# Optimization experiments

Hardware: AMD Instinct MI355X
Metric: run time of the kernel (lower is better)

The kernel has to match this reference:

```python
import jax, jax.numpy as jnp
import numpy as np

N_NODES = 50000
N_EDGES = 800000
OUT_DIM = 394
BN_EPS = 1e-5


def setup_inputs() -> dict:
    key = jax.random.key(0)
    ks = jax.random.split(key, 10)
    x = jax.random.normal(ks[0], (N_NODES, 2), dtype=jnp.float32)
    edge_index = jax.random.randint(ks[1], (2, N_EDGES), 0, N_NODES, dtype=jnp.int64)
    W_gcn = jax.random.normal(ks[2], (OUT_DIM, 2), dtype=jnp.float32) * 0.5
    b_gcn = jax.random.normal(ks[3], (OUT_DIM,), dtype=jnp.float32) * 0.1
    bn_gamma = jax.random.normal(ks[4], (OUT_DIM,), dtype=jnp.float32) * 0.1 + 1.0
    bn_beta = jax.random.normal(ks[5], (OUT_DIM,), dtype=jnp.float32) * 0.1
    bn_mean = jax.random.normal(ks[6], (OUT_DIM,), dtype=jnp.float32) * 0.1
    bn_var = jax.random.uniform(ks[7], (OUT_DIM,), dtype=jnp.float32, minval=0.5, maxval=1.5)
    fc_w = jax.random.normal(ks[8], (OUT_DIM, OUT_DIM), dtype=jnp.float32) * (1.0 / np.sqrt(OUT_DIM))
    fc_b = jax.random.normal(ks[9], (OUT_DIM,), dtype=jnp.float32) * 0.1
    return {"x": x, "edge_index": edge_index, "W_gcn": W_gcn, "b_gcn": b_gcn,
            "bn_gamma": bn_gamma, "bn_beta": bn_beta, "bn_mean": bn_mean,
            "bn_var": bn_var, "fc_w": fc_w, "fc_b": fc_b}


def reference(x, edge_index, W_gcn, b_gcn, bn_gamma, bn_beta, bn_mean, bn_var, fc_w, fc_b):
    n = x.shape[0]
    loop = jnp.arange(n, dtype=edge_index.dtype)
    # PyG GCNConv: add self-loops, symmetric deg^{-1/2} normalization
    src = jnp.concatenate([edge_index[0], loop])  # [E+N] message sources
    dst = jnp.concatenate([edge_index[1], loop])  # [E+N] message targets
    deg = jax.ops.segment_sum(jnp.ones_like(dst, dtype=x.dtype), dst, num_segments=n)
    dinv = jnp.where(deg > 0, jax.lax.rsqrt(deg), 0.0)
    norm = dinv[src] * dinv[dst]  # [E+N]
    xl = x @ W_gcn.T  # [N, 394] linear transform before aggregation
    msgs = xl[src] * norm[:, None]  # [E+N, 394] gathered + normalized messages
    agg = jax.ops.segment_sum(msgs, dst, num_segments=n) + b_gcn  # scatter-add
    h = jax.nn.relu(agg)
    # BatchNorm1d in eval mode (running stats)
    h = (h - bn_mean) * jax.lax.rsqrt(bn_var + BN_EPS) * bn_gamma + bn_beta
    # dropout is a no-op in eval mode
    z = h @ fc_w.T + fc_b
    return (jax.nn.log_softmax(z, axis=1), z)
```

## Files before the change

### kernel.cpp

```cpp
#include <hip/hip_runtime.h>
#include <math.h>

#define DIM 394
#define KP  416
#define NT  13
#define NP  448
#define BN_EPS 1e-5f
#define MAXD 32
#define TST 452

typedef __bf16 bf16x8 __attribute__((ext_vector_type(8)));
typedef float  f32x4  __attribute__((ext_vector_type(4)));

__device__ inline bool edges_are_int32(const int* ei) {
    int l = threadIdx.x & 63;
    unsigned long long b = __ballot(ei[2 * l + 1] != 0);
    return b != 0ULL;
}


__global__ void prep_kernel(const float* __restrict__ Wg, const float* __restrict__ bg,
                            const float* __restrict__ gamma, const float* __restrict__ beta,
                            const float* __restrict__ mean, const float* __restrict__ var,
                            const float* __restrict__ fcw,
                            uint4* __restrict__ zbase, float4* __restrict__ Pk,
                            float* __restrict__ Ok, bf16x8* __restrict__ Bp,
                            int z4, int zb) {
    int b = blockIdx.x, t = threadIdx.x;
    if (b < zb) {
        int i = b * 256 + t;
        if (i < z4) zbase[i] = make_uint4(0u, 0u, 0u, 0u);
    } else if (b < zb + 2) {
        int k = (b - zb) * 256 + t;
        if (k < KP) {
            float4 p = make_float4(0.f, 0.f, 0.f, 0.f);
            float o = 0.f;
            if (k < DIM) {
                p.x = Wg[2 * k];
                p.y = Wg[2 * k + 1];
                p.z = bg[k];
                float sc = gamma[k] * rsqrtf(var[k] + BN_EPS);
                p.w = sc;
                o = beta[k] - sc * mean[k];
            }
            Pk[k] = p;
            Ok[k] = o;
        }
    } else {
        int idx = (b - zb - 2) * 256 + t;
        if (idx < NT * 4 * NP) {
            int col = idx % NP;
            int r   = idx / NP;
            int k0  = r * 8;
            bf16x8 v;
            #pragma unroll
            for (int q = 0; q < 8; ++q) {
                int k = k0 + q;
                float f = (col < DIM && k < DIM) ? fcw[col * DIM + k] : 0.0f;
                v[q] = (__bf16)f;
            }
            Bp[idx] = v;
        }
    }
}

__global__ void place_kernel(const int* __restrict__ ei,
                             unsigned* __restrict__ degc,
                             unsigned* __restrict__ payload,
                             unsigned* __restrict__ ocnt,
                             uint2* __restrict__ olist, int e) {
    bool is32 = edges_are_int32(ei);
    int i0 = (blockIdx.x * blockDim.x + threadIdx.x) * 16;
    if (i0 >= e) return;
    int s[16], d[16];
    int cnt = 16;
    if (i0 + 16 <= e && (e & 15) == 0) {
        if (is32) {
            #pragma unroll
            for (int v = 0; v < 4; ++v) {
                int4 a = *reinterpret_cast<const int4*>(&ei[i0 + 4 * v]);
                int4 c = *reinterpret_cast<const int4*>(&ei[e + i0 + 4 * v]);
                s[4*v] = a.x; s[4*v+1] = a.y; s[4*v+2] = a.z; s[4*v+3] = a.w;
                d[4*v] = c.x; d[4*v+1] = c.y; d[4*v+2] = c.z; d[4*v+3] = c.w;
            }
        } else {
            #pragma unroll
            for (int v = 0; v < 8; ++v) {
                int4 a = *reinterpret_cast<const int4*>(&ei[2 * i0 + 4 * v]);
                int4 c = *reinterpret_cast<const int4*>(&ei[2 * (e + i0) + 4 * v]);
                s[2*v] = a.x; s[2*v+1] = a.z;
                d[2*v] = c.x; d[2*v+1] = c.z;
            }
        }
    } else {
        cnt = e - i0 < 16 ? e - i0 : 16;
        for (int j = 0; j < cnt; ++j) {
            s[j] = is32 ? ei[i0 + j]     : ei[2 * (i0 + j)];
            d[j] = is32 ? ei[e + i0 + j] : ei[2 * (e + i0 + j)];
        }
    }
    #pragma unroll
    for (int j = 0; j < 16; ++j) {
        if (j >= cnt) break;
        unsigned tk = atomicAdd(&degc[d[j]], 1u);
        if (tk < MAXD) {
            payload[(size_t)d[j] * MAXD + tk] = (unsigned)s[j];
        } else {
            unsigned o = atomicAdd(ocnt, 1u);
            olist[o] = make_uint2((unsigned)s[j], (unsigned)d[j]);
        }
    }
}

__global__ void xs_cleanup_kernel(const float2* __restrict__ x2,
                                  const unsigned* __restrict__ degc,
                                  float2* __restrict__ xs2,
                                  const uint2* __restrict__ olist,
                                  const unsigned* __restrict__ ocnt,
                                  float* __restrict__ yover, int n, int nb0) {
    int b = blockIdx.x;
    if (b < nb0) {
        int i = b * 256 + threadIdx.x;
        if (i < n) {
            float di = rsqrtf(1.0f + (float)degc[i]);
            float2 xv = x2[i];
            xs2[i] = make_float2(di * xv.x, di * xv.y);
        }
    } else {
        unsigned cnt = *ocnt;
        unsigned t = (b - nb0) * 256 + threadIdx.x;
        for (unsigned i = t; i < cnt; i += 512) {
            uint2 sd = olist[i];
            float ds = rsqrtf(1.0f + (float)degc[sd.x]);
            float2 xv = x2[sd.x];
            atomicAdd(&yover[2 * sd.y],     ds * xv.x);
            atomicAdd(&yover[2 * sd.y + 1], ds * xv.y);
        }
    }
}

__global__ __launch_bounds__(256, 2)
void gemm_fused(const float2* __restrict__ xs2, const unsigned* __restrict__ degc,
                const unsigned* __restrict__ payload, const float* __restrict__ yover,
                const float4* __restrict__ PkG, const float* __restrict__ OkG,
                const bf16x8* __restrict__ Bp, const float* __restrict__ fcb,
                float* __restrict__ outp, float* __restrict__ z, int n) {
    __shared__ alignas(16) char smem[16 * TST * 4 + 64];
    bf16x8* As   = (bf16x8*)smem;
    float2* red  = (float2*)(smem + 8192);
    float4* PkL  = (float4*)(smem + 10240);
    float*  OkL  = (float*)(smem + 16896);
    float*  T    = (float*)smem;
    float*  lsebuf = (float*)(smem + 16 * TST * 4);

    int tid = threadIdx.x;
    int wv  = tid >> 6;
    int l   = tid & 63;
    int cg_ = tid & 15;
    int kg  = l >> 4;
    int row0 = blockIdx.x * 64;
    int gi = row0 + l;

    for (int i = tid; i < KP; i += 256) {
        PkL[i] = PkG[i];
        OkL[i] = OkG[i];
    }

    float y0 = 0.f, y1 = 0.f;
    {
        float2 psum = make_float2(0.f, 0.f);
        float dinv_i = 0.f;
        float2 xsg = make_float2(0.f, 0.f);
        if (gi < n) {
            unsigned dg = degc[gi];
            dinv_i = rsqrtf(1.0f + (float)dg);
            xsg = xs2[gi];
            unsigned m = dg < MAXD ? dg : MAXD;
            const unsigned* pl = payload + (size_t)gi * MAXD;
            for (unsigned t = wv; t < m; t += 4) {
                float2 xv = xs2[pl[t]];
                psum.x += xv.x;
                psum.y += xv.y;
            }
            if (wv == 0) {
                psum.x += yover[2 * gi];
                psum.y += yover[2 * gi + 1];
            }
        }
        red[l * 4 + wv] = psum;
        __syncthreads();
        if (gi < n) {
            float sx = red[l * 4 + 0].x + red[l * 4 + 1].x + red[l * 4 + 2].x + red[l * 4 + 3].x;
            float sy = red[l * 4 + 0].y + red[l * 4 + 1].y + red[l * 4 + 2].y + red[l * 4 + 3].y;
            y0 = dinv_i * (sx + xsg.x);
            y1 = dinv_i * (sy + xsg.y);
        }
    }

    f32x4 acc[4][7];
    #pragma unroll
    for (int a = 0; a < 4; ++a)
        #pragma unroll
        for (int b = 0; b < 7; ++b)
            acc[a][b] = (f32x4){0.f, 0.f, 0.f, 0.f};

    auto stageA = [&](int ks, int buf) {
        int kb = ks * 32 + wv * 8;
        bf16x8 hv;
        #pragma unroll
        for (int q = 0; q < 8; ++q) {
            float4 p = PkL[kb + q];
            float t = fmaf(y0, p.x, fmaf(y1, p.y, p.z));
            t = fmaxf(t, 0.f);
            hv[q] = (__bf16)fmaf(p.w, t, OkL[kb + q]);
        }
        As[buf * 256 + wv * 64 + l] = hv;
    };

    const bf16x8* bptr = Bp + (kg * 448 + wv * 112 + cg_);

    bf16x8 Bcur[7], Bnxt[7];
    #pragma unroll
    for (int c = 0; c < 7; ++c) Bcur[c] = bptr[c * 16];
    stageA(0, 0);
    __syncthreads();

    int buf = 0;
    for (int ks = 0; ks < NT; ++ks) {
        if (ks < NT - 1) {
            const bf16x8* bn = bptr + (size_t)(ks + 1) * (4 * 448);
            #pragma unroll
            for (int c = 0; c < 7; ++c) Bnxt[c] = bn[c * 16];
            stageA(ks + 1, buf ^ 1);
        }
        bf16x8 af[4];
        #pragma unroll
        for (int rt = 0; rt < 4; ++rt)
            af[rt] = As[buf * 256 + kg * 64 + rt * 16 + cg_];
        #pragma unroll
        for (int ct = 0; ct < 7; ++ct)
            #pragma unroll
            for (int rt = 0; rt < 4; ++rt)
                acc[rt][ct] = __builtin_amdgcn_mfma_f32_16x16x32_bf16(
                                  af[rt], Bcur[ct], acc[rt][ct], 0, 0, 0);
        __syncthreads();
        #pragma unroll
        for (int c = 0; c < 7; ++c) Bcur[c] = Bnxt[c];
        buf ^= 1;
    }

    float* redm = (float*)smem;
    float* reds = redm + 256;

    int colb = wv * 112;
    float bias[7];
    bool  cv[7];
    #pragma unroll
    for (int ct = 0; ct < 7; ++ct) {
        int c = colb + ct * 16 + cg_;
        cv[ct] = (c < DIM);
        bias[ct] = cv[ct] ? fcb[c] : 0.f;
    }
    #pragma unroll
    for (int rt = 0; rt < 4; ++rt)
        #pragma unroll
        for (int ct = 0; ct < 7; ++ct)
            acc[rt][ct] = acc[rt][ct] + bias[ct];

    f32x4 mx[4];
    #pragma unroll
    for (int rt = 0; rt < 4; ++rt) {
        f32x4 m = (f32x4){-1e30f, -1e30f, -1e30f, -1e30f};
        #pragma unroll
        for (int ct = 0; ct < 7; ++ct) {
            if (!cv[ct]) continue;
            #pragma unroll
            for (int j = 0; j < 4; ++j) m[j] = fmaxf(m[j], acc[rt][ct][j]);
        }
        #pragma unroll
        for (int msk = 1; msk < 16; msk <<= 1)
            #pragma unroll
            for (int j = 0; j < 4; ++j)
                m[j] = fmaxf(m[j], __shfl_xor(m[j], msk));
        mx[rt] = m;
    }
    __syncthreads();
    if (cg_ == 0) {
        #pragma unroll
        for (int rt = 0; rt < 4; ++rt)
            #pragma unroll
            for (int j = 0; j < 4; ++j)
                redm[(rt * 16 + kg * 4 + j) * 4 + wv] = mx[rt][j];
    }
    __syncthreads();
    f32x4 gm[4];
    #pragma unroll
    for (int rt = 0; rt < 4; ++rt)
        #pragma unroll
        for (int j = 0; j < 4; ++j) {
            int r = (rt * 16 + kg * 4 + j) * 4;
            gm[rt][j] = fmaxf(fmaxf(redm[r], redm[r + 1]),
                              fmaxf(redm[r + 2], redm[r + 3]));
        }

    f32x4 sm[4];
    #pragma unroll
    for (int rt = 0; rt < 4; ++rt) {
        f32x4 s = (f32x4){0.f, 0.f, 0.f, 0.f};
        #pragma unroll
        for (int ct = 0; ct < 7; ++ct) {
            if (!cv[ct]) continue;
            #pragma unroll
            for (int j = 0; j < 4; ++j)
                s[j] += __expf(acc[rt][ct][j] - gm[rt][j]);
        }
        #pragma unroll
        for (int msk = 1; msk < 16; msk <<= 1)
            #pragma unroll
            for (int j = 0; j < 4; ++j)
                s[j] += __shfl_xor(s[j], msk);
        sm[rt] = s;
    }
    if (cg_ == 0) {
        #pragma unroll
        for (int rt = 0; rt < 4; ++rt)
            #pragma unroll
            for (int j = 0; j < 4; ++j)
                reds[(rt * 16 + kg * 4 + j) * 4 + wv] = sm[rt][j];
    }
    __syncthreads();
    f32x4 lse[4];
    #pragma unroll
    for (int rt = 0; rt < 4; ++rt)
        #pragma unroll
        for (int j = 0; j < 4; ++j) {
            int r = (rt * 16 + kg * 4 + j) * 4;
            float t = reds[r] + reds[r + 1] + reds[r + 2] + reds[r + 3];
            lse[rt][j] = gm[rt][j] + __logf(t);
        }
    __syncthreads();

    #pragma unroll
    for (int rt = 0; rt < 4; ++rt) {
        #pragma unroll
        for (int ct = 0; ct < 7; ++ct) {
            int c = colb + ct * 16 + cg_;
            #pragma unroll
            for (int j = 0; j < 4; ++j)
                T[(kg * 4 + j) * TST + c] = acc[rt][ct][j];
        }
        if (wv == 0 && cg_ == 0) {
            #pragma unroll
            for (int j = 0; j < 4; ++j)
                lsebuf[kg * 4 + j] = lse[rt][j];
        }
        __syncthreads();
        #pragma unroll
        for (int q = 0; q < 7; ++q) {
            int idx = tid + q * 256;
            int row = idx / 112;
            int c4  = idx - row * 112;
            int grow2 = row0 + rt * 16 + row;
            if (grow2 < n && c4 <= 98) {
                float4 v = *reinterpret_cast<const float4*>(&T[row * TST + c4 * 4]);
                float L = lsebuf[row];
                size_t base = (size_t)grow2 * DIM + c4 * 4;
                if (c4 <= 97) {
                    *reinterpret_cast<float2*>(&z[base])        = make_float2(v.x, v.y);
                    *reinterpret_cast<float2*>(&z[base + 2])    = make_float2(v.z, v.w);
                    *reinterpret_cast<float2*>(&outp[base])     = make_float2(v.x - L, v.y - L);
                    *reinterpret_cast<float2*>(&outp[base + 2]) = make_float2(v.z - L, v.w - L);
                } else {
                    *reinterpret_cast<float2*>(&z[base])    = make_float2(v.x, v.y);
                    *reinterpret_cast<float2*>(&outp[base]) = make_float2(v.x - L, v.y - L);
                }
            }
        }
        __syncthreads();
    }
}

extern "C" void kernel_launch(void* const* d_in, const int* in_sizes, int n_in,
                              void* d_out, int out_size, void* d_ws, size_t ws_size,
                              hipStream_t stream) {
    int n = in_sizes[0] / 2;
    int e = in_sizes[1] / 2;

    const float2* x2   = (const float2*)d_in[0];
    const int*   ei    = (const int*)d_in[1];
    const float* Wg    = (const float*)d_in[2];
    const float* bg    = (const float*)d_in[3];
    const float* gamma = (const float*)d_in[4];
    const float* beta  = (const float*)d_in[5];
    const float* mean  = (const float*)d_in[6];
    const float* var   = (const float*)d_in[7];
    const float* fcw   = (const float*)d_in[8];
    const float* fcb   = (const float*)d_in[9];

    float* out = (float*)d_out;
    float* z   = out + (size_t)n * DIM;

    char* wsb = (char*)d_ws;
    unsigned* degc  = (unsigned*)wsb;
    float*    yover = (float*)(degc + n);
    unsigned* ocnt  = (unsigned*)(yover + 2 * (size_t)n);
    float2*   xs2   = (float2*)(ocnt + 4);
    uint2*    olist = (uint2*)(xs2 + n);
    size_t off = (size_t)(5 * n + 4) * 4 + (size_t)e * 8;
    off = (off + 255) & ~(size_t)255;
    unsigned* payload = (unsigned*)(wsb + off);
    off += (size_t)n * MAXD * 4;
    off = (off + 255) & ~(size_t)255;
    bf16x8* Bp = (bf16x8*)(wsb + off);
    off += (size_t)NT * 4 * NP * 16;
    float4* Pk = (float4*)(wsb + off);
    off += (size_t)KP * 16;
    float* Ok  = (float*)(wsb + off);

    int zwords = 3 * n + 4;
    int z4 = (zwords + 3) / 4;
    int zb = (z4 + 255) / 256;
    int prep_blocks = zb + 2 + (NT * 4 * NP + 255) / 256;
    int eb16 = (e / 16 + 255) / 256 + 1;
    int nb0 = (n + 255) / 256;

    prep_kernel<<<prep_blocks, 256, 0, stream>>>(Wg, bg, gamma, beta, mean, var,
                                                 fcw, (uint4*)degc, Pk, Ok, Bp,
                                                 z4, zb);
    place_kernel<<<eb16, 256, 0, stream>>>(ei, degc, payload, ocnt, olist, e);
    xs_cleanup_kernel<<<nb0 + 2, 256, 0, stream>>>(x2, degc, xs2, olist, ocnt,
                                                   yover, n, nb0);

    int gm = (n + 63) / 64;
    gemm_fused<<<gm, 256, 0, stream>>>(xs2, degc, payload, yover,
                                       Pk, Ok, Bp, fcb, out, z, n);
}
```

Baseline: 115.3 us.

## Shrink GEMM row tile to 32 rows and raise occupancy to four blocks per CU

The fused GCN+FC kernel now handles 32 rows per block instead of 64, halving accumulator registers, and launch bounds ask for 4 blocks per CU instead of 2. Neighbor aggregation is split across 8 partial sums per row, and A staging writes bf16x4 halves. The B register double-buffer is dropped, so B fragments are loaded at the top of each k-step. The goal is more resident waves to hide gather and load latency, at the cost of twice as many B-matrix reads per output row and less overlap of B loads within a block.

```diff
diff --git a/kernel.cpp b/kernel.cpp
--- a/kernel.cpp
+++ b/kernel.cpp
@@ -10,6 +10,7 @@
 #define TST 452
 
 typedef __bf16 bf16x8 __attribute__((ext_vector_type(8)));
+typedef __bf16 bf16x4 __attribute__((ext_vector_type(4)));
 typedef float  f32x4  __attribute__((ext_vector_type(4)));
 
 __device__ inline bool edges_are_int32(const int* ei) {
@@ -139,27 +140,31 @@
     }
 }
 
-__global__ __launch_bounds__(256, 2)
+__global__ __launch_bounds__(256, 4)
 void gemm_fused(const float2* __restrict__ xs2, const unsigned* __restrict__ degc,
                 const unsigned* __restrict__ payload, const float* __restrict__ yover,
                 const float4* __restrict__ PkG, const float* __restrict__ OkG,
                 const bf16x8* __restrict__ Bp, const float* __restrict__ fcb,
                 float* __restrict__ outp, float* __restrict__ z, int n) {
     __shared__ alignas(16) char smem[16 * TST * 4 + 64];
-    bf16x8* As   = (bf16x8*)smem;
-    float2* red  = (float2*)(smem + 8192);
-    float4* PkL  = (float4*)(smem + 10240);
-    float*  OkL  = (float*)(smem + 16896);
+    bf16x4* As4  = (bf16x4*)smem;
+    float2* red  = (float2*)(smem + 4096);
+    float4* PkL  = (float4*)(smem + 6144);
+    float*  OkL  = (float*)(smem + 12800);
     float*  T    = (float*)smem;
     float*  lsebuf = (float*)(smem + 16 * TST * 4);
 
     int tid = threadIdx.x;
     int wv  = tid >> 6;
-    int l   = tid & 63;
     int cg_ = tid & 15;
-    int kg  = l >> 4;
-    int row0 = blockIdx.x * 64;
-    int gi = row0 + l;
+    int kg  = (tid & 63) >> 4;
+    int row0 = blockIdx.x * 32;
+
+    int srow  = tid & 31;
+    int skc   = (tid >> 5) & 3;
+    int shalf = tid >> 7;
+    int p8    = tid >> 5;
+    int gi = row0 + srow;
 
     for (int i = tid; i < KP; i += 256) {
         PkL[i] = PkG[i];
@@ -177,80 +182,79 @@
             xsg = xs2[gi];
             unsigned m = dg < MAXD ? dg : MAXD;
             const unsigned* pl = payload + (size_t)gi * MAXD;
-            for (unsigned t = wv; t < m; t += 4) {
+            for (unsigned t = p8; t < m; t += 8) {
                 float2 xv = xs2[pl[t]];
                 psum.x += xv.x;
                 psum.y += xv.y;
             }
-            if (wv == 0) {
+            if (p8 == 0) {
                 psum.x += yover[2 * gi];
                 psum.y += yover[2 * gi + 1];
             }
         }
-        red[l * 4 + wv] = psum;
+        red[srow * 8 + p8] = psum;
         __syncthreads();
         if (gi < n) {
-            float sx = red[l * 4 + 0].x + red[l * 4 + 1].x + red[l * 4 + 2].x + red[l * 4 + 3].x;
-            float sy = red[l * 4 + 0].y + red[l * 4 + 1].y + red[l * 4 + 2].y + red[l * 4 + 3].y;
+            float sx = 0.f, sy = 0.f;
+            #pragma unroll
+            for (int p = 0; p < 8; ++p) {
+                sx += red[srow * 8 + p].x;
+                sy += red[srow * 8 + p].y;
+            }
             y0 = dinv_i * (sx + xsg.x);
             y1 = dinv_i * (sy + xsg.y);
         }
     }
 
-    f32x4 acc[4][7];
-    #pragma unroll
-    for (int a = 0; a < 4; ++a)
+    f32x4 acc[2][7];
+    #pragma unroll
+    for (int a = 0; a < 2; ++a)
         #pragma unroll
         for (int b = 0; b < 7; ++b)
             acc[a][b] = (f32x4){0.f, 0.f, 0.f, 0.f};
 
     auto stageA = [&](int ks, int buf) {
-        int kb = ks * 32 + wv * 8;
-        bf16x8 hv;
-        #pragma unroll
-        for (int q = 0; q < 8; ++q) {
+        int kb = ks * 32 + skc * 8 + shalf * 4;
+        bf16x4 hv;
+        #pragma unroll
+        for (int q = 0; q < 4; ++q) {
             float4 p = PkL[kb + q];
             float t = fmaf(y0, p.x, fmaf(y1, p.y, p.z));
             t = fmaxf(t, 0.f);
             hv[q] = (__bf16)fmaf(p.w, t, OkL[kb + q]);
         }
-        As[buf * 256 + wv * 64 + l] = hv;
+        As4[buf * 256 + (skc * 32 + srow) * 2 + shalf] = hv;
     };
 
     const bf16x8* bptr = Bp + (kg * 448 + wv * 112 + cg_);
 
-    bf16x8 Bcur[7], Bnxt[7];
-    #pragma unroll
-    for (int c = 0; c < 7; ++c) Bcur[c] = bptr[c * 16];
     stageA(0, 0);
     __syncthreads();
 
     int buf = 0;
     for (int ks = 0; ks < NT; ++ks) {
-        if (ks < NT - 1) {
-            const bf16x8* bn = bptr + (size_t)(ks + 1) * (4 * 448);
-            #pragma unroll
-            for (int c = 0; c < 7; ++c) Bnxt[c] = bn[c * 16];
-            stageA(ks + 1, buf ^ 1);
-        }
-        bf16x8 af[4];
-        #pragma unroll
-        for (int rt = 0; rt < 4; ++rt)
-            af[rt] = As[buf * 256 + kg * 64 + rt * 16 + cg_];
+        bf16x8 Bcur[7];
+        const bf16x8* bk = bptr + (size_t)ks * 1792;
+        #pragma unroll
+        for (int c = 0; c < 7; ++c) Bcur[c] = bk[c * 16];
+        if (ks < NT - 1) stageA(ks + 1, buf ^ 1);
+        const bf16x8* As8 = (const bf16x8*)As4 + buf * 128;
+        bf16x8 af[2];
+        #pragma unroll
+        for (int rt = 0; rt < 2; ++rt)
+            af[rt] = As8[kg * 32 + rt * 16 + cg_];
         #pragma unroll
         for (int ct = 0; ct < 7; ++ct)
             #pragma unroll
-            for (int rt = 0; rt < 4; ++rt)
+            for (int rt = 0; rt < 2; ++rt)
                 acc[rt][ct] = __builtin_amdgcn_mfma_f32_16x16x32_bf16(
                                   af[rt], Bcur[ct], acc[rt][ct], 0, 0, 0);
         __syncthreads();
-        #pragma unroll
-        for (int c = 0; c < 7; ++c) Bcur[c] = Bnxt[c];
         buf ^= 1;
     }
 
     float* redm = (float*)smem;
-    float* reds = redm + 256;
+    float* reds = redm + 128;
 
     int colb = wv * 112;
     float bias[7];
@@ -262,14 +266,14 @@
         bias[ct] = cv[ct] ? fcb[c] : 0.f;
     }
     #pragma unroll
-    for (int rt = 0; rt < 4; ++rt)
+    for (int rt = 0; rt < 2; ++rt)
         #pragma unroll
         for (int ct = 0; ct < 7; ++ct)
             acc[rt][ct] = acc[rt][ct] + bias[ct];
 
-    f32x4 mx[4];
-    #pragma unroll
-    for (int rt = 0; rt < 4; ++rt) {
+    f32x4 mx[2];
+    #pragma unroll
+    for (int rt = 0; rt < 2; ++rt) {
         f32x4 m = (f32x4){-1e30f, -1e30f, -1e30f, -1e30f};
         #pragma unroll
         for (int ct = 0; ct < 7; ++ct) {
@@ -287,15 +291,15 @@
     __syncthreads();
     if (cg_ == 0) {
         #pragma unroll
-        for (int rt = 0; rt < 4; ++rt)
+        for (int rt = 0; rt < 2; ++rt)
             #pragma unroll
             for (int j = 0; j < 4; ++j)
                 redm[(rt * 16 + kg * 4 + j) * 4 + wv] = mx[rt][j];
     }
     __syncthreads();
-    f32x4 gm[4];
-    #pragma unroll
-    for (int rt = 0; rt < 4; ++rt)
+    f32x4 gm[2];
+    #pragma unroll
+    for (int rt = 0; rt < 2; ++rt)
         #pragma unroll
         for (int j = 0; j < 4; ++j) {
             int r = (rt * 16 + kg * 4 + j) * 4;
@@ -303,9 +307,9 @@
                               fmaxf(redm[r + 2], redm[r + 3]));
         }
 
-    f32x4 sm[4];
-    #pragma unroll
-    for (int rt = 0; rt < 4; ++rt) {
+    f32x4 sm[2];
+    #pragma unroll
+    for (int rt = 0; rt < 2; ++rt) {
         f32x4 s = (f32x4){0.f, 0.f, 0.f, 0.f};
         #pragma unroll
         for (int ct = 0; ct < 7; ++ct) {
@@ -323,15 +327,15 @@
     }
     if (cg_ == 0) {
         #pragma unroll
-        for (int rt = 0; rt < 4; ++rt)
+        for (int rt = 0; rt < 2; ++rt)
             #pragma unroll
             for (int j = 0; j < 4; ++j)
                 reds[(rt * 16 + kg * 4 + j) * 4 + wv] = sm[rt][j];
     }
     __syncthreads();
-    f32x4 lse[4];
-    #pragma unroll
-    for (int rt = 0; rt < 4; ++rt)
+    f32x4 lse[2];
+    #pragma unroll
+    for (int rt = 0; rt < 2; ++rt)
         #pragma unroll
         for (int j = 0; j < 4; ++j) {
             int r = (rt * 16 + kg * 4 + j) * 4;
@@ -341,7 +345,7 @@
     __syncthreads();
 
     #pragma unroll
-    for (int rt = 0; rt < 4; ++rt) {
+    for (int rt = 0; rt < 2; ++rt) {
         #pragma unroll
         for (int ct = 0; ct < 7; ++ct) {
             int c = colb + ct * 16 + cg_;
@@ -431,7 +435,7 @@
     xs_cleanup_kernel<<<nb0 + 2, 256, 0, stream>>>(x2, degc, xs2, olist, ocnt,
                                                    yover, n, nb0);
 
-    int gm = (n + 63) / 64;
+    int gm = (n + 31) / 32;
     gemm_fused<<<gm, 256, 0, stream>>>(xs2, degc, payload, yover,
                                        Pk, Ok, Bp, fcb, out, z, n);
 }
```

Result: no change. 114.7 us (median of 2 runs) (-0.5%).
